# Performance work log

Measured on AMD Instinct MI355X. Metric: run time of the kernel, lower is better.

## Reference

```python
import jax, jax.numpy as jnp
import numpy as np

B, N, IN_FT, OUT_FT = 1, 8192, 512, 256


def setup_inputs() -> dict:
    key = jax.random.key(0)
    k1, k2, k3, k4 = jax.random.split(key, 4)
    features = jax.random.normal(k1, (B, N, IN_FT), dtype=jnp.float32)
    adj = jax.random.uniform(k2, (B, N, N), dtype=jnp.float32)
    aug_adj1 = jax.random.uniform(k3, (B, N, N), dtype=jnp.float32)
    # Linear weight (xavier uniform), no bias on the Linear itself
    limit = float(np.sqrt(6.0 / (IN_FT + OUT_FT)))
    W = jax.random.uniform(k4, (OUT_FT, IN_FT), dtype=jnp.float32, minval=-limit, maxval=limit)
    bias = jnp.zeros((OUT_FT,), dtype=jnp.float32)  # GCN bias, filled 0
    prelu_a = jnp.full((1,), 0.25, dtype=jnp.float32)  # PReLU default slope
    return {"features": features, "adj": adj, "aug_adj1": aug_adj1,
            "W": W, "bias": bias, "prelu_a": prelu_a, "sparse": 0}


def _prelu(x, a):
    return jnp.where(x >= 0, x, a * x)


def _gcn(features, adj, W, bias, prelu_a):
    # Linear (no bias): [B,N,in] x [out,in]^T -> [B,N,out]
    seq_fts = jnp.einsum('bni,oi->bno', features, W)
    # Dense adjacency aggregation: bmm(adj, seq_fts)
    out = jnp.einsum('bnm,bmo->bno', adj, seq_fts) + bias
    return _prelu(out, prelu_a)


def reference(features, adj, aug_adj1, W, bias, prelu_a, sparse):
    # sparse flag is static (0 -> dense bmm path)
    h_0 = _gcn(features, adj, W, bias, prelu_a)
    h_1 = _gcn(features, aug_adj1, W, bias, prelu_a)
    return (h_0, h_1)
```

## Files before the change

### kernel.cpp

```cpp
#include <hip/hip_runtime.h>

#define NROW 8192
#define INF  512
#define OUTF 256
#define M_ELEM (NROW * OUTF)
#define NSTEP 64

typedef __bf16 v8bf __attribute__((ext_vector_type(8)));
typedef __bf16 v4bf __attribute__((ext_vector_type(4)));
typedef float  v4f  __attribute__((ext_vector_type(4)));
typedef float  v2f  __attribute__((ext_vector_type(2)));

__device__ __forceinline__ v8bf cvt_bf8(v4f u0, v4f u1) {
  v8bf v;
  v[0]=(__bf16)u0[0]; v[1]=(__bf16)u0[1]; v[2]=(__bf16)u0[2]; v[3]=(__bf16)u0[3];
  v[4]=(__bf16)u1[0]; v[5]=(__bf16)u1[1]; v[6]=(__bf16)u1[2]; v[7]=(__bf16)u1[3];
  return v;
}

__global__ __launch_bounds__(256) void seq_fts_kernel(
    const float* __restrict__ feat, const float* __restrict__ W,
    __bf16* __restrict__ Bp) {
  const int tid  = threadIdx.x;
  const int lane = tid & 63, w = tid >> 6;
  const int llo  = lane & 15, lhi = lane >> 4;
  const int row0 = blockIdx.x * 64;
  const int col0 = w * 64;

  v4f acc[4][4] = {};
#pragma unroll 1
  for (int kb = 0; kb < INF / 32; ++kb) {
    const int kofs = kb * 32 + lhi * 8;
    v8bf a[4], b[4];
#pragma unroll
    for (int i = 0; i < 4; ++i) {
      const float* p = feat + (size_t)(row0 + i * 16 + llo) * INF + kofs;
      a[i] = cvt_bf8(*(const v4f*)p, *(const v4f*)(p + 4));
    }
#pragma unroll
    for (int i = 0; i < 4; ++i) {
      const float* p = W + (size_t)(col0 + i * 16 + llo) * INF + kofs;
      b[i] = cvt_bf8(*(const v4f*)p, *(const v4f*)(p + 4));
    }
#pragma unroll
    for (int ri = 0; ri < 4; ++ri)
#pragma unroll
      for (int ci = 0; ci < 4; ++ci)
        acc[ri][ci] = __builtin_amdgcn_mfma_f32_16x16x32_bf16(
            a[ri], b[ci], acc[ri][ci], 0, 0, 0);
  }
#pragma unroll
  for (int ri = 0; ri < 4; ++ri)
#pragma unroll
    for (int ci = 0; ci < 4; ++ci) {
      const int mf = row0 + ri * 16 + lhi * 4;
      const int o  = col0 + ci * 16 + llo;
      size_t e = (((size_t)(mf >> 5) * 16 + (o >> 4)) * 64 +
                  ((mf >> 3) & 3) * 16 + (o & 15)) * 8 + (mf & 7);
      v4bf v;
      v[0] = (__bf16)acc[ri][ci][0]; v[1] = (__bf16)acc[ri][ci][1];
      v[2] = (__bf16)acc[ri][ci][2]; v[3] = (__bf16)acc[ri][ci][3];
      *(v4bf*)(Bp + e) = v;
    }
}

__global__ __launch_bounds__(512, 2) void gcn_agg_kernel(
    const float* __restrict__ adjA, const float* __restrict__ adjB,
    const __bf16* __restrict__ Bp, const float* __restrict__ bias,
    const float* __restrict__ prelu_a, float* __restrict__ out) {
  const int tid  = threadIdx.x;
  const int lane = tid & 63, w = tid >> 6;
  const int llo  = lane & 15, lhi = lane >> 4;
  const int row0 = blockIdx.x * 64;
  const int z    = blockIdx.y;
  const float* __restrict__ adj = z ? adjB : adjA;

  __shared__ __align__(16) char LdsA[2][32768];

  v4f acc[4][2] = {};

  v2f areg[8];
  auto issue_a = [&](int t) {
#pragma unroll
    for (int i = 0; i < 8; ++i) {
      const int r = w * 8 + i;
      const float* src =
          adj + (size_t)(row0 + r) * NROW + t * 128 + (lane << 1);
      areg[i] = __builtin_nontemporal_load((const v2f*)src);
    }
  };
  auto write_a = [&](int buf) {
#pragma unroll
    for (int i = 0; i < 8; ++i) {
      const int r   = w * 8 + i;
      const int key = ((r & 15) << 1) | ((r >> 3) & 1);
      const int byt = r * 512 + ((((lane >> 1) ^ key) << 4) | ((lane & 1) << 3));
      *(v2f*)(&LdsA[buf][byt]) = areg[i];
    }
  };

  const __bf16* __restrict__ Bpw = Bp + ((size_t)(w * 2) * 64 + lane) * 8;
  v8bf b[4][2];
  auto load_b_all = [&](int t) {
#pragma unroll
    for (int g = 0; g < 4; ++g)
#pragma unroll
      for (int ci = 0; ci < 2; ++ci)
        b[g][ci] = *(const v8bf*)(
            Bpw + ((size_t)((t * 4 + g) * 16 + ci)) * 512);
  };

  auto compute_g = [&](int buf, int kg) {
    const char* ab = &LdsA[buf][0];
    v8bf af[4];
#pragma unroll
    for (int rt = 0; rt < 4; ++rt) {
      const int r   = rt * 16 + llo;
      const int key = ((r & 15) << 1) | ((r >> 3) & 1);
      const char* base = ab + r * 512;
      const int s0 = kg * 8 + lhi * 2;
      v4f u0 = *(const v4f*)(base + (((s0    ) ^ key) << 4));
      v4f u1 = *(const v4f*)(base + (((s0 + 1) ^ key) << 4));
      af[rt] = cvt_bf8(u0, u1);
    }
#pragma unroll
    for (int ci = 0; ci < 2; ++ci)
#pragma unroll
      for (int rt = 0; rt < 4; ++rt)
        acc[rt][ci] = __builtin_amdgcn_mfma_f32_16x16x32_bf16(
            af[rt], b[kg][ci], acc[rt][ci], 0, 0, 0);
  };

  issue_a(0);
  asm volatile("s_waitcnt vmcnt(0)" ::: "memory");
  write_a(0);
  asm volatile("s_waitcnt lgkmcnt(0)" ::: "memory");
  __builtin_amdgcn_s_barrier();

#pragma unroll 1
  for (int t = 0; t < NSTEP; ++t) {
    load_b_all(t);
    __builtin_amdgcn_sched_barrier(0);
    if (t + 1 < NSTEP) issue_a(t + 1);
    __builtin_amdgcn_sched_barrier(0);
#pragma unroll
    for (int kg = 0; kg < 4; ++kg)
      compute_g(t & 1, kg);
    __builtin_amdgcn_sched_barrier(0);
    if (t + 1 < NSTEP) {
      asm volatile("s_waitcnt vmcnt(0)" ::: "memory");
      write_a((t + 1) & 1);
      asm volatile("s_waitcnt lgkmcnt(0)" ::: "memory");
    }
    __builtin_amdgcn_s_barrier();
  }

  const float slope = prelu_a[0];
  float* __restrict__ outp = out + (size_t)z * M_ELEM;
#pragma unroll
  for (int ci = 0; ci < 2; ++ci) {
    const int o  = w * 32 + ci * 16 + llo;
    const float bs = bias[o];
#pragma unroll
    for (int rt = 0; rt < 4; ++rt) {
      const int m = row0 + rt * 16 + lhi * 4;
#pragma unroll
      for (int r = 0; r < 4; ++r) {
        float v = acc[rt][ci][r] + bs;
        outp[(size_t)(m + r) * OUTF + o] = v >= 0.f ? v : slope * v;
      }
    }
  }
}

extern "C" void kernel_launch(void* const* d_in, const int* in_sizes, int n_in,
                              void* d_out, int out_size, void* d_ws, size_t ws_size,
                              hipStream_t stream) {
  const float* feat = (const float*)d_in[0];
  const float* adj  = (const float*)d_in[1];
  const float* aug  = (const float*)d_in[2];
  const float* W    = (const float*)d_in[3];
  const float* bias = (const float*)d_in[4];
  const float* pa   = (const float*)d_in[5];
  float* out = (float*)d_out;
  __bf16* Bp = (__bf16*)d_ws;

  seq_fts_kernel<<<dim3(NROW / 64), 256, 0, stream>>>(feat, W, Bp);
  gcn_agg_kernel<<<dim3(NROW / 64, 2), 512, 0, stream>>>(
      adj, aug, Bp, bias, pa, out);
}
```

Measured before the change: 205.4 us.

## Halve row tile and deepen adjacency/feature prefetch to two stages ahead

Both kernels now use 32-row tiles instead of 64, doubling the grid size. The aggregation kernel drops per-step vmcnt(0) waits and instead keeps two register sets for adjacency and B fragments, issuing loads two steps ahead. Each global load then has a full compute phase to land before its data is written to LDS. The smaller tile halves LDS use and raises block count and occupancy. In exchange it doubles total reads of the B matrix and holds more registers for the in-flight buffers.

Result: faster. 183.9 us (-10.4%).

```diff
diff --git a/kernel.cpp b/kernel.cpp
--- a/kernel.cpp
+++ b/kernel.cpp
@@ -24,16 +24,16 @@
   const int tid  = threadIdx.x;
   const int lane = tid & 63, w = tid >> 6;
   const int llo  = lane & 15, lhi = lane >> 4;
-  const int row0 = blockIdx.x * 64;
+  const int row0 = blockIdx.x * 32;
   const int col0 = w * 64;
 
-  v4f acc[4][4] = {};
+  v4f acc[2][4] = {};
 #pragma unroll 1
   for (int kb = 0; kb < INF / 32; ++kb) {
     const int kofs = kb * 32 + lhi * 8;
-    v8bf a[4], b[4];
+    v8bf a[2], b[4];
 #pragma unroll
-    for (int i = 0; i < 4; ++i) {
+    for (int i = 0; i < 2; ++i) {
       const float* p = feat + (size_t)(row0 + i * 16 + llo) * INF + kofs;
       a[i] = cvt_bf8(*(const v4f*)p, *(const v4f*)(p + 4));
     }
@@ -43,14 +43,14 @@
       b[i] = cvt_bf8(*(const v4f*)p, *(const v4f*)(p + 4));
     }
 #pragma unroll
-    for (int ri = 0; ri < 4; ++ri)
+    for (int ri = 0; ri < 2; ++ri)
 #pragma unroll
       for (int ci = 0; ci < 4; ++ci)
         acc[ri][ci] = __builtin_amdgcn_mfma_f32_16x16x32_bf16(
             a[ri], b[ci], acc[ri][ci], 0, 0, 0);
   }
 #pragma unroll
-  for (int ri = 0; ri < 4; ++ri)
+  for (int ri = 0; ri < 2; ++ri)
 #pragma unroll
     for (int ci = 0; ci < 4; ++ci) {
       const int mf = row0 + ri * 16 + lhi * 4;
@@ -71,37 +71,37 @@
   const int tid  = threadIdx.x;
   const int lane = tid & 63, w = tid >> 6;
   const int llo  = lane & 15, lhi = lane >> 4;
-  const int row0 = blockIdx.x * 64;
+  const int row0 = blockIdx.x * 32;
   const int z    = blockIdx.y;
   const float* __restrict__ adj = z ? adjB : adjA;
 
-  __shared__ __align__(16) char LdsA[2][32768];
+  __shared__ __align__(16) char LdsA[2][16384];
 
-  v4f acc[4][2] = {};
+  v4f acc[2][2] = {};
 
-  v2f areg[8];
-  auto issue_a = [&](int t) {
+  v2f aS0[4], aS1[4];
+  auto issue_a = [&](int t, v2f (&ar)[4]) {
 #pragma unroll
-    for (int i = 0; i < 8; ++i) {
-      const int r = w * 8 + i;
+    for (int i = 0; i < 4; ++i) {
+      const int r = w * 4 + i;
       const float* src =
           adj + (size_t)(row0 + r) * NROW + t * 128 + (lane << 1);
-      areg[i] = __builtin_nontemporal_load((const v2f*)src);
+      ar[i] = __builtin_nontemporal_load((const v2f*)src);
     }
   };
-  auto write_a = [&](int buf) {
+  auto write_a = [&](int buf, v2f (&ar)[4]) {
 #pragma unroll
-    for (int i = 0; i < 8; ++i) {
-      const int r   = w * 8 + i;
+    for (int i = 0; i < 4; ++i) {
+      const int r   = w * 4 + i;
       const int key = ((r & 15) << 1) | ((r >> 3) & 1);
       const int byt = r * 512 + ((((lane >> 1) ^ key) << 4) | ((lane & 1) << 3));
-      *(v2f*)(&LdsA[buf][byt]) = areg[i];
+      *(v2f*)(&LdsA[buf][byt]) = ar[i];
     }
   };
 
   const __bf16* __restrict__ Bpw = Bp + ((size_t)(w * 2) * 64 + lane) * 8;
-  v8bf b[4][2];
-  auto load_b_all = [&](int t) {
+  v8bf bS0[4][2], bS1[4][2];
+  auto issue_b = [&](int t, v8bf (&b)[4][2]) {
 #pragma unroll
     for (int g = 0; g < 4; ++g)
 #pragma unroll
@@ -110,46 +110,51 @@
             Bpw + ((size_t)((t * 4 + g) * 16 + ci)) * 512);
   };
 
-  auto compute_g = [&](int buf, int kg) {
+  auto compute = [&](int buf, v8bf (&b)[4][2]) {
     const char* ab = &LdsA[buf][0];
-    v8bf af[4];
 #pragma unroll
-    for (int rt = 0; rt < 4; ++rt) {
-      const int r   = rt * 16 + llo;
-      const int key = ((r & 15) << 1) | ((r >> 3) & 1);
-      const char* base = ab + r * 512;
-      const int s0 = kg * 8 + lhi * 2;
-      v4f u0 = *(const v4f*)(base + (((s0    ) ^ key) << 4));
-      v4f u1 = *(const v4f*)(base + (((s0 + 1) ^ key) << 4));
-      af[rt] = cvt_bf8(u0, u1);
+    for (int kg = 0; kg < 4; ++kg) {
+      v8bf af[2];
+#pragma unroll
+      for (int rt = 0; rt < 2; ++rt) {
+        const int r   = rt * 16 + llo;
+        const int key = ((r & 15) << 1) | ((r >> 3) & 1);
+        const char* base = ab + r * 512;
+        const int s0 = kg * 8 + lhi * 2;
+        v4f u0 = *(const v4f*)(base + (((s0    ) ^ key) << 4));
+        v4f u1 = *(const v4f*)(base + (((s0 + 1) ^ key) << 4));
+        af[rt] = cvt_bf8(u0, u1);
+      }
+#pragma unroll
+      for (int ci = 0; ci < 2; ++ci)
+#pragma unroll
+        for (int rt = 0; rt < 2; ++rt)
+          acc[rt][ci] = __builtin_amdgcn_mfma_f32_16x16x32_bf16(
+              af[rt], b[kg][ci], acc[rt][ci], 0, 0, 0);
     }
-#pragma unroll
-    for (int ci = 0; ci < 2; ++ci)
-#pragma unroll
-      for (int rt = 0; rt < 4; ++rt)
-        acc[rt][ci] = __builtin_amdgcn_mfma_f32_16x16x32_bf16(
-            af[rt], b[kg][ci], acc[rt][ci], 0, 0, 0);
   };
 
-  issue_a(0);
-  asm volatile("s_waitcnt vmcnt(0)" ::: "memory");
-  write_a(0);
+  issue_a(0, aS0);
+  issue_b(0, bS0);
+  issue_a(1, aS1);
+  issue_b(1, bS1);
+  write_a(0, aS0);
   asm volatile("s_waitcnt lgkmcnt(0)" ::: "memory");
   __builtin_amdgcn_s_barrier();
 
 #pragma unroll 1
-  for (int t = 0; t < NSTEP; ++t) {
-    load_b_all(t);
-    __builtin_amdgcn_sched_barrier(0);
-    if (t + 1 < NSTEP) issue_a(t + 1);
-    __builtin_amdgcn_sched_barrier(0);
-#pragma unroll
-    for (int kg = 0; kg < 4; ++kg)
-      compute_g(t & 1, kg);
-    __builtin_amdgcn_sched_barrier(0);
-    if (t + 1 < NSTEP) {
-      asm volatile("s_waitcnt vmcnt(0)" ::: "memory");
-      write_a((t + 1) & 1);
+  for (int u = 0; u < NSTEP; u += 2) {
+    if (u + 2 < NSTEP) issue_a(u + 2, aS0);
+    compute(0, bS0);
+    if (u + 2 < NSTEP) issue_b(u + 2, bS0);
+    write_a(1, aS1);
+    asm volatile("s_waitcnt lgkmcnt(0)" ::: "memory");
+    __builtin_amdgcn_s_barrier();
+    if (u + 3 < NSTEP) issue_a(u + 3, aS1);
+    compute(1, bS1);
+    if (u + 3 < NSTEP) issue_b(u + 3, bS1);
+    if (u + 2 < NSTEP) {
+      write_a(0, aS0);
       asm volatile("s_waitcnt lgkmcnt(0)" ::: "memory");
     }
     __builtin_amdgcn_s_barrier();
@@ -162,7 +167,7 @@
     const int o  = w * 32 + ci * 16 + llo;
     const float bs = bias[o];
 #pragma unroll
-    for (int rt = 0; rt < 4; ++rt) {
+    for (int rt = 0; rt < 2; ++rt) {
       const int m = row0 + rt * 16 + lhi * 4;
 #pragma unroll
       for (int r = 0; r < 4; ++r) {
@@ -185,7 +190,7 @@
   float* out = (float*)d_out;
   __bf16* Bp = (__bf16*)d_ws;
 
-  seq_fts_kernel<<<dim3(NROW / 64), 256, 0, stream>>>(feat, W, Bp);
-  gcn_agg_kernel<<<dim3(NROW / 64, 2), 512, 0, stream>>>(
+  seq_fts_kernel<<<dim3(NROW / 32), 256, 0, stream>>>(feat, W, Bp);
+  gcn_agg_kernel<<<dim3(NROW / 32, 2), 512, 0, stream>>>(
       adj, aug, Bp, bias, pa, out);
 }
```
